# Optimization experiments

Measured on AMD Instinct MI355X. Metric: run time of the kernel, lower is better.

The kernel has to match this reference:

```python
import jax, jax.numpy as jnp
import numpy as np
from jax import lax

HIDDEN = 7168
Q_LORA = 1536
N_HEAD = 64
HEAD_DIM = 128
ROPE_DIM = 64
TOPK = 2048
T = 4096
ROPE_BASE = 10000.0
LN_EPS = 1e-6
NEG_INF = -1e30


def _apply_rope_interleaved(x, cos, sin):
    # x: [..., ROPE_DIM], cos/sin broadcastable to [..., ROPE_DIM//2]
    x1 = x[..., 0::2]
    x2 = x[..., 1::2]
    o1 = x1 * cos - x2 * sin
    o2 = x1 * sin + x2 * cos
    out = jnp.stack([o1, o2], axis=-1)  # interleave back
    return out.reshape(x.shape)


def setup_inputs() -> dict:
    key = jax.random.key(0)
    ks = jax.random.split(key, 6)
    hidden_states = jax.random.normal(ks[0], (T, HIDDEN), dtype=jnp.float32)
    qr = jax.random.normal(ks[1], (T, Q_LORA), dtype=jnp.float32)
    positions = jnp.arange(T, dtype=jnp.int32)
    # learned parameters (stored [in, out] so fwd is x @ W)
    Wq_b = jax.random.normal(ks[2], (Q_LORA, N_HEAD * HEAD_DIM), dtype=jnp.float32) * 0.02
    Wk = jax.random.normal(ks[3], (HIDDEN, HEAD_DIM), dtype=jnp.float32) * 0.02
    Wproj = jax.random.normal(ks[4], (HIDDEN, N_HEAD), dtype=jnp.float32) * 0.02
    k_norm_gamma = jnp.ones((HEAD_DIM,), dtype=jnp.float32)
    k_norm_beta = jnp.zeros((HEAD_DIM,), dtype=jnp.float32)
    return {
        'hidden_states': hidden_states,
        'qr': qr,
        'positions': positions,
        'Wq_b': Wq_b,
        'Wk': Wk,
        'Wproj': Wproj,
        'k_norm_gamma': k_norm_gamma,
        'k_norm_beta': k_norm_beta,
    }


def _indexer_forward(hidden_states, qr, positions, Wq_b, Wk, Wproj, gamma, beta):
    # q projection: [T, n_head * head_dim] -> [T, H, D]
    q = (qr @ Wq_b).reshape(T, N_HEAD, HEAD_DIM)
    q_pe, q_nope = q[..., :ROPE_DIM], q[..., ROPE_DIM:]

    # k projection + LayerNorm (eps=1e-6)
    k = hidden_states @ Wk  # [T, D]
    mu = jnp.mean(k, axis=-1, keepdims=True)
    var = jnp.mean(jnp.square(k - mu), axis=-1, keepdims=True)
    k = (k - mu) * lax.rsqrt(var + LN_EPS) * gamma + beta
    k_pe, k_nope = k[..., :ROPE_DIM], k[..., ROPE_DIM:]

    # RoPE (interleaved / GPT-J style, as used by DeepSeek rotary)
    inv_freq = 1.0 / (ROPE_BASE ** (jnp.arange(0, ROPE_DIM, 2, dtype=jnp.float32) / ROPE_DIM))
    ang = positions.astype(jnp.float32)[:, None] * inv_freq[None, :]  # [T, R/2]
    cos, sin = jnp.cos(ang), jnp.sin(ang)
    q_pe = _apply_rope_interleaved(q_pe, cos[:, None, :], sin[:, None, :])  # [T, H, R]
    k_pe = _apply_rope_interleaved(k_pe, cos, sin)  # [T, R]

    q_full = jnp.concatenate([q_pe, q_nope], axis=-1)  # [T, H, D]
    k_full = jnp.concatenate([k_pe, k_nope], axis=-1)  # [T, D]

    # per-token per-head weights, scaled by head_dim**-0.5 * n_head**-0.5
    w = (hidden_states @ Wproj) * (HEAD_DIM ** -0.5) * (N_HEAD ** -0.5)  # [T, H]

    # lightning-indexer score: sum_h w[t,h] * relu(q[t,h,:] . k[s,:])
    # scan over heads so live intermediate is a single [T, T] matrix
    qh_all = jnp.transpose(q_full, (1, 0, 2))  # [H, T, D]
    wh_all = w.T  # [H, T]

    def body(acc, hw):
        qh, wh = hw  # [T, D], [T]
        acc = acc + wh[:, None] * jax.nn.relu(qh @ k_full.T)
        return acc, None

    scores, _ = lax.scan(body, jnp.zeros((T, T), dtype=jnp.float32), (qh_all, wh_all))

    # causal mask over key positions, then select top-k keys per query
    causal = positions[:, None] >= positions[None, :]
    masked = jnp.where(causal, scores, NEG_INF)
    topk_vals, topk_idx = lax.top_k(masked, TOPK)  # [T, TOPK]
    return topk_vals, topk_idx


def reference(hidden_states, qr, positions, Wq_b, Wk, Wproj, k_norm_gamma, k_norm_beta):
    return _indexer_forward(hidden_states, qr, positions, Wq_b, Wk, Wproj, k_norm_gamma, k_norm_beta)
```

## Files before the change

kernel.cpp:

```cpp
#include <hip/hip_runtime.h>
#include <stdint.h>

#define TT 4096
#define HID 7168
#define QL 1536
#define NH 64
#define HD 128
#define QD 8192
#define KTOP 2048
#define WSCALE 0.011048543456039806f

typedef _Float16 f16;
typedef uint16_t u16;
typedef unsigned u32;
typedef __attribute__((ext_vector_type(4))) float f32x4;
typedef __attribute__((ext_vector_type(16))) float f32x16;
typedef __attribute__((ext_vector_type(8))) _Float16 f16x8;
typedef __attribute__((ext_vector_type(4))) _Float16 f16x4;

__device__ __forceinline__ void lds_load16(const void* g, void* l) {
  __builtin_amdgcn_global_load_lds(
      (const __attribute__((address_space(1))) unsigned*)g,
      (__attribute__((address_space(3))) unsigned*)l, 16, 0, 0);
}

__device__ __forceinline__ u16 f16_bits(f16 h) {
  union { f16 h; u16 u; } c; c.h = h; return c.u;
}
__device__ __forceinline__ float f16_from_bits(u16 u) {
  union { u16 u; f16 h; } c; c.u = u; return (float)c.h;
}

__device__ __forceinline__ size_t soff(int t) {
  int b = t >> 7, r = t & 127;
  return (size_t)128u * ((size_t)(b + 1) * (size_t)(64 * b + r));
}

__global__ void tcvt(const float* __restrict__ in, f16* __restrict__ out,
                     int R, int C, int ostride, int orow0) {
  __shared__ float tile[32][33];
  int cb = blockIdx.x * 32, rb = blockIdx.y * 32;
  int tx = threadIdx.x & 31, ty = threadIdx.x >> 5;
  for (int i = 0; i < 32; i += 8)
    tile[ty + i][tx] = in[(size_t)(rb + ty + i) * C + cb + tx];
  __syncthreads();
  for (int i = 0; i < 32; i += 8)
    out[(size_t)(cb + ty + i + orow0) * ostride + rb + tx] = (f16)tile[tx][ty + i];
}

__launch_bounds__(256, 2)
__global__ void gemm_q(const float* __restrict__ A, const f16* __restrict__ B, f16* __restrict__ C) {
  __shared__ __align__(16) f16 As[128 * 32];
  __shared__ __align__(16) f16 Bs[128 * 32];
  int tid = threadIdx.x, lane = tid & 63, wave = tid >> 6;
  int bm = blockIdx.y << 7, bn = blockIdx.x << 7;
  int wm = (wave & 1) << 6, wn = (wave >> 1) << 6;
  const f16* gb = B + (size_t)(bn + (tid >> 2)) * QL + (tid & 3) * 8;
  f16* lB = Bs + wave * 512;
  int ar = tid >> 3, ac = (tid & 7) * 4;
  f32x4 acc[4][4] = {};
  for (int k0 = 0; k0 < QL; k0 += 32) {
    __syncthreads();
#pragma unroll
    for (int i = 0; i < 4; i++) {
      float4 v = *(const float4*)(A + (size_t)(bm + ar + i * 32) * QL + k0 + ac);
      f16x4 h = {(f16)v.x, (f16)v.y, (f16)v.z, (f16)v.w};
      *(f16x4*)(As + (ar + i * 32) * 32 + ac) = h;
    }
    lds_load16(gb + k0, lB);
    lds_load16(gb + (size_t)64 * QL + k0, lB + 2048);
    __syncthreads();
    int ro = lane & 15, ko = (lane >> 4) << 3;
    f16x8 af[4], bf[4];
#pragma unroll
    for (int i = 0; i < 4; i++) af[i] = *(const f16x8*)(As + (wm + i * 16 + ro) * 32 + ko);
#pragma unroll
    for (int i = 0; i < 4; i++) bf[i] = *(const f16x8*)(Bs + (wn + i * 16 + ro) * 32 + ko);
#pragma unroll
    for (int mi = 0; mi < 4; mi++)
#pragma unroll
      for (int ni = 0; ni < 4; ni++)
        acc[mi][ni] = __builtin_amdgcn_mfma_f32_16x16x32_f16(af[mi], bf[ni], acc[mi][ni], 0, 0, 0);
  }
  int cr = (lane >> 4) << 2, cc = lane & 15;
#pragma unroll
  for (int mi = 0; mi < 4; mi++)
#pragma unroll
    for (int ni = 0; ni < 4; ni++) {
      int row = bm + wm + mi * 16 + cr;
      int col = bn + wn + ni * 16 + cc;
      f16* cp = C + (size_t)row * QD + col;
#pragma unroll
      for (int r = 0; r < 4; r++) cp[(size_t)r * QD] = (f16)acc[mi][ni][r];
    }
}

__launch_bounds__(256, 2)
__global__ void gemm_kw(const float* __restrict__ A, const f16* __restrict__ B,
                        float* __restrict__ kraw, float* __restrict__ wout) {
  __shared__ __align__(16) f16 As[64 * 64];
  __shared__ __align__(16) f16 Bs[64 * 64];
  int tid = threadIdx.x, lane = tid & 63, wave = tid >> 6;
  int bm = blockIdx.y << 6, bn = blockIdx.x << 6;
  int wm = (wave & 1) << 5, wn = (wave >> 1) << 5;
  const f16* gb = B + (size_t)(bn + (tid >> 3)) * HID + (tid & 7) * 8;
  f16* lB = Bs + wave * 512;
  int ar = tid >> 4, ac = (tid & 15) * 4;
  f32x4 acc[2][2] = {};
  for (int k0 = 0; k0 < HID; k0 += 64) {
    __syncthreads();
#pragma unroll
    for (int i = 0; i < 4; i++) {
      float4 v = *(const float4*)(A + (size_t)(bm + ar + i * 16) * HID + k0 + ac);
      f16x4 h = {(f16)v.x, (f16)v.y, (f16)v.z, (f16)v.w};
      *(f16x4*)(As + (ar + i * 16) * 64 + ac) = h;
    }
    lds_load16(gb + k0, lB);
    lds_load16(gb + (size_t)32 * HID + k0, lB + 2048);
    __syncthreads();
    int ro = lane & 15, ko = (lane >> 4) << 3;
    f16x8 af[2][2], bf[2][2];
#pragma unroll
    for (int i = 0; i < 2; i++)
#pragma unroll
      for (int kk = 0; kk < 2; kk++) {
        af[i][kk] = *(const f16x8*)(As + (wm + i * 16 + ro) * 64 + kk * 32 + ko);
        bf[i][kk] = *(const f16x8*)(Bs + (wn + i * 16 + ro) * 64 + kk * 32 + ko);
      }
#pragma unroll
    for (int mi = 0; mi < 2; mi++)
#pragma unroll
      for (int ni = 0; ni < 2; ni++)
#pragma unroll
        for (int kk = 0; kk < 2; kk++)
          acc[mi][ni] = __builtin_amdgcn_mfma_f32_16x16x32_f16(af[mi][kk], bf[ni][kk], acc[mi][ni], 0, 0, 0);
  }
  int cr = (lane >> 4) << 2, cc = lane & 15;
#pragma unroll
  for (int mi = 0; mi < 2; mi++)
#pragma unroll
    for (int ni = 0; ni < 2; ni++) {
      int row = bm + wm + mi * 16 + cr;
      int col = bn + wn + ni * 16 + cc;
#pragma unroll
      for (int r = 0; r < 4; r++) {
        float v = acc[mi][ni][r];
        int rr = row + r;
        if (col < HD) kraw[(size_t)rr * HD + col] = v;
        else          wout[(size_t)rr * NH + (col - HD)] = v * WSCALE;
      }
    }
}

__global__ void ln_rope(const float* __restrict__ kraw, const int* __restrict__ pos,
                        const float* __restrict__ gamma, const float* __restrict__ beta,
                        f16* __restrict__ k16) {
  int row = (blockIdx.x << 2) + (threadIdx.x >> 6);
  int lane = threadIdx.x & 63;
  const float* kr = kraw + (size_t)row * HD;
  float2 x = ((const float2*)kr)[lane];
  float s = x.x + x.y, s2 = x.x * x.x + x.y * x.y;
  for (int off = 32; off; off >>= 1) { s += __shfl_down(s, off); s2 += __shfl_down(s2, off); }
  s = __shfl(s, 0); s2 = __shfl(s2, 0);
  float mu = s * (1.f / 128.f);
  float var = s2 * (1.f / 128.f) - mu * mu;
  float inv = rsqrtf(var + 1e-6f);
  float y0 = (x.x - mu) * inv * gamma[lane * 2] + beta[lane * 2];
  float y1 = (x.y - mu) * inv * gamma[lane * 2 + 1] + beta[lane * 2 + 1];
  float o0 = y0, o1 = y1;
  if (lane < 32) {
    float p = (float)pos[row];
    float invf = exp2f(-(float)lane * 0.41524101185942813f);
    float ang = p * invf;
    float sn, cn;
    sincosf(ang, &sn, &cn);
    o0 = y0 * cn - y1 * sn;
    o1 = y0 * sn + y1 * cn;
  }
  k16[(size_t)row * HD + 2 * lane] = (f16)o0;
  k16[(size_t)row * HD + 2 * lane + 1] = (f16)o1;
}

__global__ void rope_q(f16* __restrict__ q16, const int* __restrict__ pos) {
  int t = blockIdx.x, tid = threadIdx.x;
  __shared__ float cs[64];
  if (tid < 32) {
    float invf = exp2f(-(float)tid * 0.41524101185942813f);
    float ang = (float)pos[t] * invf;
    float sn, cn;
    sincosf(ang, &sn, &cn);
    cs[tid] = cn;
    cs[32 + tid] = sn;
  }
  __syncthreads();
  f16* row = q16 + (size_t)t * QD;
#pragma unroll
  for (int it = 0; it < 2; it++) {
    int u = it * 256 + tid;
    int h = u >> 3, c = u & 7;
    f16* p = row + h * HD + c * 8;
    f16x8 v = *(f16x8*)p;
#pragma unroll
    for (int j = 0; j < 4; j++) {
      int l = c * 4 + j;
      float cn = cs[l], sn = cs[32 + l];
      float x = (float)v[2 * j], y = (float)v[2 * j + 1];
      v[2 * j] = (f16)(x * cn - y * sn);
      v[2 * j + 1] = (f16)(x * sn + y * cn);
    }
    *(f16x8*)p = v;
  }
}

__launch_bounds__(256, 3)
__global__ void scores2(const f16* __restrict__ q16, const f16* __restrict__ k16,
                        const float* __restrict__ w, f16* __restrict__ S) {
  int bid = (int)blockIdx.x;
  bid = (bid & 7) * 136 + (bid >> 3);
  int g = 0;
  while (4 * (g + 1) * (g + 2) <= bid) g++;
  int rem = bid - 4 * g * (g + 1);
  int qt = (g << 3) + rem / (g + 1);
  int kt = rem - (rem / (g + 1)) * (g + 1);
  int kt0 = kt << 8, qt0 = qt << 5;

  int tid = threadIdx.x, l = tid & 63, wid = tid >> 6;
  int q = l & 31, half = l >> 5;
  __shared__ __align__(16) f16 smem_q[4 * 4096];
  __shared__ float w_lds[2048];

  for (int i = tid; i < 2048; i += 256) {
    int hh = i & 63, qq = i >> 6;
    w_lds[hh * 32 + qq] = w[(size_t)(qt0 + qq) * NH + hh];
  }
  f16x8 kfr[2][8];
  {
    const f16* kb = k16 + (size_t)(kt0 + wid * 64 + q) * HD + half * 8;
#pragma unroll
    for (int mt = 0; mt < 2; mt++)
#pragma unroll
      for (int kk = 0; kk < 8; kk++)
        kfr[mt][kk] = *(const f16x8*)(kb + mt * 32 * HD + kk * 16);
  }
  __syncthreads();
  asm volatile("s_waitcnt vmcnt(0)" ::: "memory");

  const f16* qbase = q16 + (size_t)qt0 * QD;
  auto stage = [&](int h) {
    const f16* src = qbase + h * HD;
    f16* dst = smem_q + (h & 3) * 4096;
#pragma unroll
    for (int p = 0; p < 2; p++) {
      int u = p * 256 + tid;
      lds_load16(src + (size_t)(u & 31) * QD + (u >> 5) * 8, dst + u * 8);
    }
  };

  f32x16 s0 = {}, s1 = {};
  auto compute = [&](int h) {
    const f16* qb = smem_q + (h & 3) * 4096;
    f32x16 a0 = {}, a1 = {};
    __builtin_amdgcn_s_setprio(1);
#pragma unroll
    for (int kk = 0; kk < 8; kk++) {
      f16x8 qf = *(const f16x8*)(qb + ((kk * 2 + half) * 32 + q) * 8);
      a0 = __builtin_amdgcn_mfma_f32_32x32x16_f16(kfr[0][kk], qf, a0, 0, 0, 0);
      a1 = __builtin_amdgcn_mfma_f32_32x32x16_f16(kfr[1][kk], qf, a1, 0, 0, 0);
    }
    __builtin_amdgcn_s_setprio(0);
    float wv = w_lds[h * 32 + q];
#pragma unroll
    for (int r = 0; r < 16; r++) {
      s0[r] += wv * fmaxf(a0[r], 0.f);
      s1[r] += wv * fmaxf(a1[r], 0.f);
    }
  };

  stage(0); stage(1); stage(2);
  for (int h = 0; h < 61; h++) {
    asm volatile("s_waitcnt vmcnt(4)" ::: "memory");
    __builtin_amdgcn_s_barrier();
    asm volatile("" ::: "memory");
    stage(h + 3);
    compute(h);
  }
  asm volatile("s_waitcnt vmcnt(4)" ::: "memory");
  __builtin_amdgcn_s_barrier();
  asm volatile("" ::: "memory");
  compute(61);
  asm volatile("s_waitcnt vmcnt(2)" ::: "memory");
  __builtin_amdgcn_s_barrier();
  asm volatile("" ::: "memory");
  compute(62);
  asm volatile("s_waitcnt vmcnt(0)" ::: "memory");
  __builtin_amdgcn_s_barrier();
  asm volatile("" ::: "memory");
  compute(63);

  f16* st = smem_q;
#pragma unroll
  for (int mt = 0; mt < 2; mt++)
#pragma unroll
    for (int r = 0; r < 16; r++) {
      int m = (r & 3) + ((r >> 2) << 3) + half * 4;
      int sl = wid * 64 + mt * 32 + m;
      float v = mt ? s1[r] : s0[r];
      if (!(v == v)) v = 0.f;
      v = fminf(fmaxf(v, -60000.f), 60000.f);
      u32 byte = (u32)(q * 512 + sl * 2) ^ (u32)((q & 7) << 4);
      *(f16*)((char*)st + byte) = (f16)v;
    }
  __syncthreads();
  {
    int rq = tid >> 3, c = tid & 7;
    int t = qt0 + rq;
    size_t base = soff(t) + (size_t)kt0;
    bool hi = (t - kt0) >= 128;
#pragma unroll
    for (int j = 0; j < 4; j++) {
      if (c < 4 || hi) {
        u32 byte = (u32)(rq * 512 + c * 64 + j * 16) ^ (u32)((rq & 7) << 4);
        uint4 v = *(uint4*)((char*)st + byte);
        *(uint4*)(S + base + c * 32 + j * 8) = v;
      }
    }
  }
}

template <int N>
__device__ __forceinline__ void sort_and_store(u32* key, int tid, int t, float* out) {
  constexpr int V = N / 256;
  u32 v[V];
#pragma unroll
  for (int r = 0; r < V; r += 4) {
    uint4 q4 = *(const uint4*)(key + tid * V + r);
    v[r] = ~q4.x; v[r + 1] = ~q4.y; v[r + 2] = ~q4.z; v[r + 3] = ~q4.w;
  }
#pragma unroll
  for (int k = 2; k <= N; k <<= 1) {
#pragma unroll
    for (int j = k >> 1; j > 0; j >>= 1) {
      if (j >= 64 * V) {
#pragma unroll
        for (int r = 0; r < V; r += 4) {
          uint4 q4 = {v[r], v[r + 1], v[r + 2], v[r + 3]};
          *(uint4*)(key + tid * V + r) = q4;
        }
        __syncthreads();
        for (int m = tid; m < N / 2; m += 256) {
          int i = ((m & ~(j - 1)) << 1) | (m & (j - 1));
          int l = i | j;
          bool up = ((i & k) == 0);
          u32 a = key[i], b = key[l];
          if (up ? (a > b) : (a < b)) { key[i] = b; key[l] = a; }
        }
        __syncthreads();
#pragma unroll
        for (int r = 0; r < V; r += 4) {
          uint4 q4 = *(const uint4*)(key + tid * V + r);
          v[r] = q4.x; v[r + 1] = q4.y; v[r + 2] = q4.z; v[r + 3] = q4.w;
        }
      } else if (j >= V) {
        int lanej = j / V;
        bool takeMin = (((tid & lanej) == 0) == (((tid * V) & k) == 0));
#pragma unroll
        for (int r = 0; r < V; r++) {
          u32 o = __shfl_xor(v[r], lanej, 64);
          u32 mn = min(v[r], o), mx = max(v[r], o);
          v[r] = takeMin ? mn : mx;
        }
      } else {
#pragma unroll
        for (int r = 0; r < V; r++) {
          if ((r & j) == 0) {
            bool up = (((tid * V + r) & k) == 0);
            u32 a = v[r], b = v[r | j];
            u32 mn = min(a, b), mx = max(a, b);
            v[r] = up ? mn : mx;
            v[r | j] = up ? mx : mn;
          }
        }
      }
    }
  }
  if (tid * V < KTOP) {
    float* ov = out + (size_t)t * KTOP + tid * V;
    float* oi = out + (size_t)TT * KTOP + (size_t)t * KTOP + tid * V;
#pragma unroll
    for (int r = 0; r < V; r++) {
      u32 kv = ~v[r];
      u32 mono = kv >> 16;
      float val;
      if (mono == 0u) {
        val = -1e30f;
      } else {
        u16 hb = (u16)((mono & 0x8000u) ? (mono ^ 0x8000u) : (mono ^ 0xFFFFu));
        val = f16_from_bits(hb);
      }
      ov[r] = val;
      oi[r] = (float)(0xFFFFu - (kv & 0xFFFFu));
    }
  }
}

__launch_bounds__(256, 4)
__global__ void topk_k(const f16* __restrict__ S, float* __restrict__ out) {
  int t = blockIdx.x, tid = threadIdx.x;
  __shared__ __align__(16) u32 key[4096];
  size_t base = soff(t);
  int nsort = (t <= 2047) ? 2048 : 4096;
  const uint4* src = (const uint4*)(S + base);
  for (int i = tid; i < (nsort >> 3); i += 256) {
    uint4 v4 = src[i];
    u32 ww[4] = {v4.x, v4.y, v4.z, v4.w};
#pragma unroll
    for (int j = 0; j < 8; j++) {
      int s = i * 8 + j;
      u32 kk;
      if (s > t) {
        kk = 0xFFFFu - (u32)s;
      } else {
        u16 hb = (u16)(ww[j >> 1] >> ((j & 1) * 16));
        u32 mono = (hb & 0x8000u) ? (u32)(hb ^ 0xFFFFu) : (u32)(hb | 0x8000u);
        kk = (mono << 16) | (0xFFFFu - (u32)s);
      }
      key[s] = kk;
    }
  }
  __syncthreads();
  if (t <= 2047) sort_and_store<2048>(key, tid, t, out);
  else           sort_and_store<4096>(key, tid, t, out);
}

extern "C" void kernel_launch(void* const* d_in, const int* in_sizes, int n_in,
                              void* d_out, int out_size, void* d_ws, size_t ws_size,
                              hipStream_t stream) {
  const float* hs = (const float*)d_in[0];
  const float* qr = (const float*)d_in[1];
  const int* pos = (const int*)d_in[2];
  const float* Wq = (const float*)d_in[3];
  const float* Wk = (const float*)d_in[4];
  const float* Wp = (const float*)d_in[5];
  const float* gamma = (const float*)d_in[6];
  const float* beta = (const float*)d_in[7];
  char* ws = (char*)d_ws;
  float* kraw = (float*)ws;
  float* wsc = (float*)(ws + 2097152);
  f16* k16 = (f16*)(ws + 3145728);
  f16* kwT = (f16*)(ws + 4194304);
  f16* wqT = (f16*)(ws + 6946816);
  f16* q16 = (f16*)(ws + 32112640);
  f16* S = (f16*)(ws + 4194304);

  tcvt<<<dim3(256, 48), dim3(256), 0, stream>>>(Wq, wqT, QL, QD, QL, 0);
  tcvt<<<dim3(4, 224), dim3(256), 0, stream>>>(Wk, kwT, HID, HD, HID, 0);
  tcvt<<<dim3(2, 224), dim3(256), 0, stream>>>(Wp, kwT, HID, NH, HID, HD);
  gemm_kw<<<dim3(3, 64), dim3(256), 0, stream>>>(hs, kwT, kraw, wsc);
  ln_rope<<<dim3(1024), dim3(256), 0, stream>>>(kraw, pos, gamma, beta, k16);
  gemm_q<<<dim3(64, 32), dim3(256), 0, stream>>>(qr, wqT, q16);
  rope_q<<<dim3(4096), dim3(256), 0, stream>>>(q16, pos);
  scores2<<<dim3(1088), dim3(256), 0, stream>>>(q16, k16, wsc, S);
  topk_k<<<dim3(4096), dim3(256), 0, stream>>>(S, (float*)d_out);
}
```

Measured before the change: 813.5 us.

## Widen scores key tile from 256 to 384 keys per block

The scores kernel now gives each block 384 keys instead of 256, so each wave keeps three 32-row K fragments in registers and issues three MFMAs per staged Q slice. The causal triangular block enumeration and XCD swizzle are recomputed for the new tile shape, with clamped K row loads and a chunked causal store. This amortizes each staged Q head slice over more MFMA work and cuts the block count. In exchange it raises register pressure (launch bounds drop to 2 blocks per CU) and adds wasted work on partial diagonal tiles.

After: 839.7 us. 1.03x slower.

```diff
diff --git a/kernel.cpp b/kernel.cpp
--- a/kernel.cpp
+++ b/kernel.cpp
@@ -212,17 +212,18 @@
   }
 }
 
-__launch_bounds__(256, 3)
-__global__ void scores2(const f16* __restrict__ q16, const f16* __restrict__ k16,
+__launch_bounds__(256, 2)
+__global__ void scores3(const f16* __restrict__ q16, const f16* __restrict__ k16,
                         const float* __restrict__ w, f16* __restrict__ S) {
-  int bid = (int)blockIdx.x;
-  bid = (bid & 7) * 136 + (bid >> 3);
+  int raw = (int)blockIdx.x;
+  int x = raw & 7, i0 = raw >> 3;
+  int bid = (x < 4 ? x * 94 : 4 * 94 + (x - 4) * 93) + i0;
   int g = 0;
-  while (4 * (g + 1) * (g + 2) <= bid) g++;
-  int rem = bid - 4 * g * (g + 1);
-  int qt = (g << 3) + rem / (g + 1);
+  while (6 * (g + 1) * (g + 2) <= bid) g++;
+  int rem = bid - 6 * g * (g + 1);
+  int qt = 12 * g + rem / (g + 1);
   int kt = rem - (rem / (g + 1)) * (g + 1);
-  int kt0 = kt << 8, qt0 = qt << 5;
+  int kb0 = kt * 384, qt0 = qt << 5;
 
   int tid = threadIdx.x, l = tid & 63, wid = tid >> 6;
   int q = l & 31, half = l >> 5;
@@ -233,14 +234,15 @@
     int hh = i & 63, qq = i >> 6;
     w_lds[hh * 32 + qq] = w[(size_t)(qt0 + qq) * NH + hh];
   }
-  f16x8 kfr[2][8];
-  {
-    const f16* kb = k16 + (size_t)(kt0 + wid * 64 + q) * HD + half * 8;
-#pragma unroll
-    for (int mt = 0; mt < 2; mt++)
-#pragma unroll
-      for (int kk = 0; kk < 8; kk++)
-        kfr[mt][kk] = *(const f16x8*)(kb + mt * 32 * HD + kk * 16);
+  f16x8 kfr[3][8];
+#pragma unroll
+  for (int mt = 0; mt < 3; mt++) {
+    int krow = kb0 + wid * 96 + mt * 32 + q;
+    if (krow > TT - 1) krow = TT - 1;
+    const f16* kb = k16 + (size_t)krow * HD + half * 8;
+#pragma unroll
+    for (int kk = 0; kk < 8; kk++)
+      kfr[mt][kk] = *(const f16x8*)(kb + kk * 16);
   }
   __syncthreads();
   asm volatile("s_waitcnt vmcnt(0)" ::: "memory");
@@ -256,23 +258,25 @@
     }
   };
 
-  f32x16 s0 = {}, s1 = {};
+  f32x16 s0 = {}, s1 = {}, s2 = {};
   auto compute = [&](int h) {
     const f16* qb = smem_q + (h & 3) * 4096;
-    f32x16 a0 = {}, a1 = {};
+    float wv = w_lds[h * 32 + q];
+    f32x16 a0 = {}, a1 = {}, a2 = {};
     __builtin_amdgcn_s_setprio(1);
 #pragma unroll
     for (int kk = 0; kk < 8; kk++) {
       f16x8 qf = *(const f16x8*)(qb + ((kk * 2 + half) * 32 + q) * 8);
       a0 = __builtin_amdgcn_mfma_f32_32x32x16_f16(kfr[0][kk], qf, a0, 0, 0, 0);
       a1 = __builtin_amdgcn_mfma_f32_32x32x16_f16(kfr[1][kk], qf, a1, 0, 0, 0);
+      a2 = __builtin_amdgcn_mfma_f32_32x32x16_f16(kfr[2][kk], qf, a2, 0, 0, 0);
     }
     __builtin_amdgcn_s_setprio(0);
-    float wv = w_lds[h * 32 + q];
 #pragma unroll
     for (int r = 0; r < 16; r++) {
       s0[r] += wv * fmaxf(a0[r], 0.f);
       s1[r] += wv * fmaxf(a1[r], 0.f);
+      s2[r] += wv * fmaxf(a2[r], 0.f);
     }
   };
 
@@ -298,30 +302,31 @@
   compute(63);
 
   f16* st = smem_q;
-#pragma unroll
-  for (int mt = 0; mt < 2; mt++)
+  auto dump = [&](const f32x16& sv, int mtile) {
 #pragma unroll
     for (int r = 0; r < 16; r++) {
       int m = (r & 3) + ((r >> 2) << 3) + half * 4;
-      int sl = wid * 64 + mt * 32 + m;
-      float v = mt ? s1[r] : s0[r];
+      int sl = wid * 96 + mtile * 32 + m;
+      float v = sv[r];
       if (!(v == v)) v = 0.f;
       v = fminf(fmaxf(v, -60000.f), 60000.f);
-      u32 byte = (u32)(q * 512 + sl * 2) ^ (u32)((q & 7) << 4);
+      u32 byte = (u32)(q * 768 + sl * 2) ^ (u32)((q & 7) << 4);
       *(f16*)((char*)st + byte) = (f16)v;
     }
+  };
+  dump(s0, 0); dump(s1, 1); dump(s2, 2);
   __syncthreads();
   {
     int rq = tid >> 3, c = tid & 7;
     int t = qt0 + rq;
-    size_t base = soff(t) + (size_t)kt0;
-    bool hi = (t - kt0) >= 128;
-#pragma unroll
-    for (int j = 0; j < 4; j++) {
-      if (c < 4 || hi) {
-        u32 byte = (u32)(rq * 512 + c * 64 + j * 16) ^ (u32)((rq & 7) << 4);
-        uint4 v = *(uint4*)((char*)st + byte);
-        *(uint4*)(S + base + c * 32 + j * 8) = v;
+    size_t base = soff(t) + (size_t)kb0;
+#pragma unroll
+    for (int j = 0; j < 6; j++) {
+      int idx16 = j * 8 + c;
+      int chunk = idx16 >> 4;
+      if (kb0 + chunk * 128 <= t) {
+        u32 byte = (u32)(rq * 768 + idx16 * 16) ^ (u32)((rq & 7) << 4);
+        *(uint4*)(S + base + idx16 * 8) = *(uint4*)((char*)st + byte);
       }
     }
   }
@@ -459,6 +464,6 @@
   ln_rope<<<dim3(1024), dim3(256), 0, stream>>>(kraw, pos, gamma, beta, k16);
   gemm_q<<<dim3(64, 32), dim3(256), 0, stream>>>(qr, wqT, q16);
   rope_q<<<dim3(4096), dim3(256), 0, stream>>>(q16, pos);
-  scores2<<<dim3(1088), dim3(256), 0, stream>>>(q16, k16, wsc, S);
+  scores3<<<dim3(748), dim3(256), 0, stream>>>(q16, k16, wsc, S);
   topk_k<<<dim3(4096), dim3(256), 0, stream>>>(S, (float*)d_out);
 }
```
